# Optimization experiments

Measured on AMD Instinct MI355X. Metric: run time of the kernel, lower is better.

## Reference

```python
import jax, jax.numpy as jnp
import numpy as np

VOCAB = 32000
HID = 1024
CUTOFFS = [0, 10000, 20000, 32000]
N_CLUSTERS = 2
DIV = 4
PROJ_DIMS = [HID // DIV**i for i in range(N_CLUSTERS + 1)]  # [1024, 256, 64]
# Faithful to source quirk: n_vocabs = cutoffs[i] + cutoffs[i+1]
LOGIT_DIMS = [CUTOFFS[i] + CUTOFFS[i + 1] for i in range(N_CLUSTERS + 1)]  # [10000, 30000, 52000]


def setup_inputs() -> dict:
    key = jax.random.key(0)
    ks = jax.random.split(key, 16)
    N = 2048
    inp = {
        "x": jax.random.normal(ks[0], (N, HID), dtype=jnp.float32),
        "y": jax.random.randint(ks[1], (N,), 0, VOCAB, dtype=jnp.int64),
    }
    s = 0.02
    # projections: Linear(hidden, proj_dims[i], bias=False); stored as [in, out]
    inp["Wp0"] = jax.random.normal(ks[2], (HID, PROJ_DIMS[0]), dtype=jnp.float32) * s
    inp["Wp1"] = jax.random.normal(ks[3], (HID, PROJ_DIMS[1]), dtype=jnp.float32) * s
    inp["Wp2"] = jax.random.normal(ks[4], (HID, PROJ_DIMS[2]), dtype=jnp.float32) * s
    # logits: Linear(proj_dims[i], LOGIT_DIMS[i]) with bias
    inp["Wl0"] = jax.random.normal(ks[5], (PROJ_DIMS[0], LOGIT_DIMS[0]), dtype=jnp.float32) * s
    inp["bl0"] = jnp.zeros((LOGIT_DIMS[0],), dtype=jnp.float32)
    inp["Wl1"] = jax.random.normal(ks[6], (PROJ_DIMS[1], LOGIT_DIMS[1]), dtype=jnp.float32) * s
    inp["bl1"] = jnp.zeros((LOGIT_DIMS[1],), dtype=jnp.float32)
    inp["Wl2"] = jax.random.normal(ks[7], (PROJ_DIMS[2], LOGIT_DIMS[2]), dtype=jnp.float32) * s
    inp["bl2"] = jnp.zeros((LOGIT_DIMS[2],), dtype=jnp.float32)
    # cluster_logit: Linear(hidden, n_clusters)
    inp["Wc"] = jax.random.normal(ks[8], (HID, N_CLUSTERS), dtype=jnp.float32) * s
    inp["bc"] = jnp.zeros((N_CLUSTERS,), dtype=jnp.float32)
    return inp


def reference(x, y, Wp0, Wp1, Wp2, Wl0, bl0, Wl1, bl1, Wl2, bl2, Wc, bc):
    # head: project (dim-preserving here) then head-vocab logits + cluster logits
    head_proj = x @ Wp0                                   # [N, 1024]
    head_logit = jnp.concatenate(
        [head_proj @ Wl0 + bl0, head_proj @ Wc + bc], axis=1
    )                                                     # [N, 10000 + 2]
    head_lp = jax.nn.log_softmax(head_logit, axis=1)

    nll = jnp.zeros(y.shape, dtype=x.dtype)

    # cluster 0: targets in [0, cutoffs[1])
    m0 = (y >= CUTOFFS[0]) & (y < CUTOFFS[1])
    t0 = jnp.clip(y - CUTOFFS[0], 0, head_lp.shape[1] - 1)
    lp0 = jnp.take_along_axis(head_lp, t0[:, None], axis=1)[:, 0]
    nll = jnp.where(m0, -lp0, nll)

    # tail clusters: small projection GEMM + log_softmax + gather, combined via masks
    tails = [(Wp1, Wl1, bl1), (Wp2, Wl2, bl2)]
    for i, (Wp, Wl, bl) in enumerate(tails, start=1):
        l, r = CUTOFFS[i], CUTOFFS[i + 1]
        mask = (y >= l) & (y < r)
        t = jnp.clip(y - l, 0, Wl.shape[1] - 1)
        tail_lp = jax.nn.log_softmax((x @ Wp) @ Wl + bl, axis=1)  # [N, LOGIT_DIMS[i]]
        # faithful to source: head column -i (reversed cluster order quirk)
        lp = head_lp[:, -i] + jnp.take_along_axis(tail_lp, t[:, None], axis=1)[:, 0]
        nll = jnp.where(mask, -lp, nll)

    return nll
```

## Files before the change

kernel.cpp:

```cpp
#include <hip/hip_runtime.h>
#include <math.h>

#define HID 1024
#define NROWS 2048

typedef __attribute__((ext_vector_type(8))) short short8;
typedef __attribute__((ext_vector_type(4))) short short4_t;
typedef __attribute__((ext_vector_type(4))) float f32x4;

__device__ __forceinline__ short f2bf(float f) {
  union { float f; unsigned u; } v; v.f = f;
  unsigned r = v.u + 0x7fffu + ((v.u >> 16) & 1u);
  return (short)(r >> 16);
}
__device__ __forceinline__ float bf2f(short s) {
  union { unsigned u; float f; } v; v.u = ((unsigned)(unsigned short)s) << 16;
  return v.f;
}
__device__ __forceinline__ float wave_sum(float a) {
#pragma unroll
  for (int off = 32; off; off >>= 1) a += __shfl_xor(a, off, 64);
  return a;
}

__global__ __launch_bounds__(256) void prep(
    const float* __restrict__ x, const int* __restrict__ y,
    const float* __restrict__ Wp0, const float* __restrict__ Wp1,
    const float* __restrict__ Wp2, const float* __restrict__ Wl0,
    const float* __restrict__ Wl1, const float* __restrict__ Wl2,
    short* __restrict__ xb,
    int* __restrict__ counts, int* __restrict__ slot_of_row,
    int* __restrict__ rows1, int* __restrict__ rows2,
    short* __restrict__ T0, short* __restrict__ T1, short* __restrict__ T2,
    short* __restrict__ T3, short* __restrict__ T4, short* __restrict__ T5) {
  const int tid = threadIdx.x;
  int b = blockIdx.x;
  if (b == 0) {
    __shared__ int c1s, c2s;
    if (tid == 0) { c1s = 0; c2s = 0; }
    __syncthreads();
    for (int r = tid; r < NROWS; r += 256) {
      const int yy = y[r];
      if (yy >= 20000) {
        const int s = atomicAdd(&c2s, 1);
        slot_of_row[r] = s; rows2[s] = r;
      } else if (yy >= 10000) {
        const int s = atomicAdd(&c1s, 1);
        slot_of_row[r] = s; rows1[s] = r;
      } else {
        slot_of_row[r] = -1;
      }
    }
    __syncthreads();
    if (tid == 0) { counts[0] = NROWS; counts[1] = c1s; counts[2] = c2s; }
    return;
  }
  if (b <= 2048) {
    const int i = ((b - 1) * 256 + tid) * 4;
    short4_t o;
    o.x = f2bf(x[i + 0]); o.y = f2bf(x[i + 1]);
    o.z = f2bf(x[i + 2]); o.w = f2bf(x[i + 3]);
    *(short4_t*)&xb[i] = o;
    return;
  }
  b -= 2049;
  const float* W; short* BT; int K, N, Npad, tn;
  if (b < 1024)                { W = Wp0; BT = T0; K = 1024; N = 1024;  Npad = 1024;  tn = 32;   }
  else if ((b -= 1024) < 256)  { W = Wp1; BT = T1; K = 1024; N = 256;   Npad = 256;   tn = 8;    }
  else if ((b -= 256) < 128)   { W = Wp2; BT = T2; K = 1024; N = 64;    Npad = 128;   tn = 4;    }
  else if ((b -= 128) < 10112) { W = Wl0; BT = T3; K = 1024; N = 10000; Npad = 10112; tn = 316;  }
  else if ((b -= 10112) < 7520){ W = Wl1; BT = T4; K = 256;  N = 30000; Npad = 30080; tn = 940;  }
  else { b -= 7520;              W = Wl2; BT = T5; K = 64;   N = 52000; Npad = 52096; tn = 1628; }

  __shared__ float T[32][33];
  const int n0 = (b % tn) * 32, k0 = (b / tn) * 32;
  const int r = tid >> 3, c = (tid & 7) * 4;
  float v0 = 0.f, v1 = 0.f, v2 = 0.f, v3 = 0.f;
  const float* p = &W[(size_t)(k0 + r) * N];
  if (n0 + c + 3 < N) {
    v0 = p[n0 + c]; v1 = p[n0 + c + 1]; v2 = p[n0 + c + 2]; v3 = p[n0 + c + 3];
  } else {
    if (n0 + c + 0 < N) v0 = p[n0 + c + 0];
    if (n0 + c + 1 < N) v1 = p[n0 + c + 1];
    if (n0 + c + 2 < N) v2 = p[n0 + c + 2];
  }
  T[r][c] = v0; T[r][c + 1] = v1; T[r][c + 2] = v2; T[r][c + 3] = v3;
  __syncthreads();
  const int nl = tid >> 3, kl = (tid & 7) * 4;
  const int n = n0 + nl;
  if (n < Npad) {
    short4_t o;
    o.x = (n < N) ? f2bf(T[kl + 0][nl]) : (short)0;
    o.y = (n < N) ? f2bf(T[kl + 1][nl]) : (short)0;
    o.z = (n < N) ? f2bf(T[kl + 2][nl]) : (short)0;
    o.w = (n < N) ? f2bf(T[kl + 3][nl]) : (short)0;
    *(short4_t*)&BT[(size_t)n * K + k0 + kl] = o;
  }
}

__device__ __forceinline__ void mfma_mainloop(const short* aB[4], const short* bB[4],
                                              short* As, short* Bs,
                                              f32x4 acc[4][4],
                                              int K, int w, int lane) {
  const int quad = lane >> 4, ln = lane & 15;
  const int wm = w >> 1, wn = w & 1;
  const int l7 = ln & 7;
  for (int kt = 0; kt < K; kt += 64) {
#pragma unroll
    for (int i = 0; i < 4; ++i) {
      const int row = w * 32 + i * 8;
      __builtin_amdgcn_global_load_lds(
          (const __attribute__((address_space(1))) void*)(aB[i] + kt),
          (__attribute__((address_space(3))) void*)(As + row * 64), 16, 0, 0);
      __builtin_amdgcn_global_load_lds(
          (const __attribute__((address_space(1))) void*)(bB[i] + kt),
          (__attribute__((address_space(3))) void*)(Bs + row * 64), 16, 0, 0);
    }
    __syncthreads();
#pragma unroll
    for (int ks = 0; ks < 2; ++ks) {
      const int kcs = ks * 4 + quad;
      short8 af[4], bfr[4];
#pragma unroll
      for (int mt = 0; mt < 4; ++mt) {
        const int row = wm * 64 + mt * 16 + ln;
        af[mt] = *(const short8*)(As + ((row * 8 + (kcs ^ l7)) << 3));
      }
#pragma unroll
      for (int nt = 0; nt < 4; ++nt) {
        const int rowb = wn * 64 + nt * 16 + ln;
        bfr[nt] = *(const short8*)(Bs + ((rowb * 8 + (kcs ^ l7)) << 3));
      }
#pragma unroll
      for (int mt = 0; mt < 4; ++mt)
#pragma unroll
        for (int nt = 0; nt < 4; ++nt)
          acc[mt][nt] = __builtin_amdgcn_mfma_f32_16x16x32_bf16(
              af[mt], bfr[nt], acc[mt][nt], 0, 0, 0);
    }
    __syncthreads();
  }
}


__global__ __launch_bounds__(256) void proj_all(
    const short* __restrict__ xb,
    const short* __restrict__ WpT0, const short* __restrict__ WpT1,
    const short* __restrict__ WpT2,
    short* __restrict__ P0b, short* __restrict__ P1c, short* __restrict__ P2c,
    const int* __restrict__ rows1, const int* __restrict__ rows2,
    const int* __restrict__ counts) {
  int b = blockIdx.x;
  const short* BT; short* C; int N, r0, c0, cnt;
  const int* rowlist = nullptr;
  if (b < 128) {
    BT = WpT0; C = P0b; N = 1024;
    c0 = (b & 7) * 128; r0 = (b >> 3) * 128; cnt = NROWS;
  } else if (b < 160) {
    b -= 128; BT = WpT1; C = P1c; N = 256;
    c0 = (b & 1) * 128; r0 = (b >> 1) * 128; rowlist = rows1; cnt = counts[1];
  } else {
    b -= 160; BT = WpT2; C = P2c; N = 64;
    c0 = 0; r0 = b * 128; rowlist = rows2; cnt = counts[2];
  }
  if (r0 >= cnt) return;

  __shared__ short As[128 * 64];
  __shared__ short Bs[128 * 64];
  const int tid = threadIdx.x;
  const int w = tid >> 6, lane = tid & 63;
  const int quad = lane >> 4, ln = lane & 15;
  const int wm = w >> 1, wn = w & 1;
  const int rsub = lane >> 3;
  const int kc = (lane & 7) ^ rsub;
  const int K = 1024;

  const short* aB[4]; const short* bB[4];
#pragma unroll
  for (int i = 0; i < 4; ++i) {
    const int sl = r0 + w * 32 + i * 8 + rsub;
    const int ar = rowlist ? rowlist[sl < cnt ? sl : cnt - 1] : sl;
    aB[i] = xb + (size_t)ar * K + kc * 8;
    bB[i] = BT + (size_t)(c0 + w * 32 + i * 8 + rsub) * K + kc * 8;
  }

  f32x4 acc[4][4];
  const f32x4 zero = {0.f, 0.f, 0.f, 0.f};
#pragma unroll
  for (int i = 0; i < 4; ++i)
#pragma unroll
    for (int j = 0; j < 4; ++j) acc[i][j] = zero;
  mfma_mainloop(aB, bB, As, Bs, acc, K, w, lane);
#pragma unroll
  for (int mt = 0; mt < 4; ++mt)
#pragma unroll
    for (int r = 0; r < 4; ++r) {
      const int grow = r0 + wm * 64 + mt * 16 + quad * 4 + r;
#pragma unroll
      for (int nt = 0; nt < 4; ++nt) {
        const int cg = c0 + wn * 64 + nt * 16 + ln;
        if (cg < N) C[(size_t)grow * N + cg] = f2bf(acc[mt][nt][r]);
      }
    }
}

#define HB  1280
#define T1B 3840
#define T2B 6528

__global__ __launch_bounds__(256) void logit_all(
    const short* __restrict__ P0b, const short* __restrict__ WlT0,
    const float* __restrict__ bl0, float* __restrict__ psh,
    const short* __restrict__ P1c, const short* __restrict__ WlT1,
    const float* __restrict__ bl1, float* __restrict__ ps1,
    const short* __restrict__ P2c, const short* __restrict__ WlT2,
    const float* __restrict__ bl2, float* __restrict__ ps2,
    const int* __restrict__ counts) {
  int b = blockIdx.x;
  const short* A; const short* BT; const float* bias; float* ps;
  int K, Ncols, nsplit, rb, cs, cnt;
  if (b < HB) {
    const int xcd = b & 7, j = b >> 3;
    rb = j / 10; cs = xcd * 10 + j % 10;
    if (cs >= 79) return;
    A = P0b; BT = WlT0; bias = bl0; ps = psh;
    K = 1024; Ncols = 10000; nsplit = 79; cnt = NROWS;
  } else if ((b -= HB) < T1B) {
    const int xcd = b & 7, j = b >> 3;
    rb = j / 30; cs = xcd * 30 + j % 30;
    if (cs >= 235) return;
    A = P1c; BT = WlT1; bias = bl1; ps = ps1;
    K = 256; Ncols = 30000; nsplit = 235; cnt = counts[1];
  } else {
    b -= T1B;
    const int xcd = b & 7, j = b >> 3;
    rb = j / 51; cs = xcd * 51 + j % 51;
    if (cs >= 407) return;
    A = P2c; BT = WlT2; bias = bl2; ps = ps2;
    K = 64; Ncols = 52000; nsplit = 407; cnt = counts[2];
  }
  const int r0 = rb * 128, c0 = cs * 128;
  if (r0 >= cnt) return;

  __shared__ short As[128 * 64];
  __shared__ short Bs[128 * 64];
  __shared__ float psL[2][128];
  const int tid = threadIdx.x;
  const int w = tid >> 6, lane = tid & 63;
  const int quad = lane >> 4, ln = lane & 15;
  const int wm = w >> 1, wn = w & 1;
  const int rsub = lane >> 3;
  const int kc = (lane & 7) ^ rsub;

  const short* aB[4]; const short* bB[4];
#pragma unroll
  for (int i = 0; i < 4; ++i) {
    aB[i] = A + (size_t)(r0 + w * 32 + i * 8 + rsub) * K + kc * 8;
    bB[i] = BT + (size_t)(c0 + w * 32 + i * 8 + rsub) * K + kc * 8;
  }

  f32x4 acc[4][4];
  const f32x4 zero = {0.f, 0.f, 0.f, 0.f};
#pragma unroll
  for (int i = 0; i < 4; ++i)
#pragma unroll
    for (int j = 0; j < 4; ++j) acc[i][j] = zero;
  mfma_mainloop(aB, bB, As, Bs, acc, K, w, lane);

  float bv[4];
#pragma unroll
  for (int nt = 0; nt < 4; ++nt) {
    const int cg = c0 + wn * 64 + nt * 16 + ln;
    bv[nt] = (cg < Ncols) ? bias[cg] : -1.0e30f;
  }
#pragma unroll
  for (int mt = 0; mt < 4; ++mt)
#pragma unroll
    for (int r = 0; r < 4; ++r) {
      float s = 0.f;
#pragma unroll
      for (int nt = 0; nt < 4; ++nt)
        s += __expf(acc[mt][nt][r] + bv[nt]);
#pragma unroll
      for (int off = 1; off < 16; off <<= 1) s += __shfl_xor(s, off, 64);
      if (ln == 0) psL[wn][wm * 64 + mt * 16 + quad * 4 + r] = s;
    }
  __syncthreads();
  if (tid < 128)
    ps[(size_t)(r0 + tid) * nsplit + cs] = psL[0][tid] + psL[1][tid];
}

__global__ __launch_bounds__(256) void finalize(
    const short* __restrict__ P0b, const short* __restrict__ P1c,
    const short* __restrict__ P2c,
    const short* __restrict__ WlT0, const float* __restrict__ bl0,
    const short* __restrict__ WlT1, const float* __restrict__ bl1,
    const short* __restrict__ WlT2, const float* __restrict__ bl2,
    const float* __restrict__ Wc, const float* __restrict__ bc,
    const int* __restrict__ y, const int* __restrict__ slot_of_row,
    const float* __restrict__ psh, const float* __restrict__ ps1,
    const float* __restrict__ ps2, float* __restrict__ out) {
  const int lane = threadIdx.x & 63;
  const int row = blockIdx.x * 4 + (threadIdx.x >> 6);

  float a0 = 0.f, a1 = 0.f;
  for (int k = lane; k < HID; k += 64) {
    const float p = bf2f(P0b[(size_t)row * HID + k]);
    a0 += p * Wc[2 * k];
    a1 += p * Wc[2 * k + 1];
  }
  a0 = wave_sum(a0);
  a1 = wave_sum(a1);
  const float cl0 = a0 + bc[0], cl1 = a1 + bc[1];

  float S = 0.f;
  for (int i = lane; i < 79; i += 64) S += psh[(size_t)row * 79 + i];
  S = wave_sum(S) + __expf(cl0) + __expf(cl1);
  const float lse = logf(S);

  const int yy = y[row];
  float nll;
  if (yy < 10000) {
    const short* pr = P0b + (size_t)row * 1024;
    const short* wr = WlT0 + (size_t)yy * 1024;
    float a = 0.f;
    for (int kk = lane * 4; kk < 1024; kk += 256) {
      const short4_t p = *(const short4_t*)(pr + kk);
      const short4_t wv = *(const short4_t*)(wr + kk);
      a += bf2f(p.x) * bf2f(wv.x) + bf2f(p.y) * bf2f(wv.y)
         + bf2f(p.z) * bf2f(wv.z) + bf2f(p.w) * bf2f(wv.w);
    }
    a = wave_sum(a);
    nll = -((a + bl0[yy]) - lse);
  } else if (yy < 20000) {
    const int t = yy - 10000;
    const int slot = slot_of_row[row];
    float S1 = 0.f;
    for (int i = lane; i < 235; i += 64) S1 += ps1[(size_t)slot * 235 + i];
    S1 = wave_sum(S1);
    const short* pr = P1c + (size_t)slot * 256;
    const short* wr = WlT1 + (size_t)t * 256;
    const int kk = lane * 4;
    const short4_t p = *(const short4_t*)(pr + kk);
    const short4_t wv = *(const short4_t*)(wr + kk);
    float a = bf2f(p.x) * bf2f(wv.x) + bf2f(p.y) * bf2f(wv.y)
            + bf2f(p.z) * bf2f(wv.z) + bf2f(p.w) * bf2f(wv.w);
    a = wave_sum(a);
    nll = -((cl1 - lse) + ((a + bl1[t]) - logf(S1)));
  } else {
    const int t = yy - 20000;
    const int slot = slot_of_row[row];
    float S2 = 0.f;
    for (int i = lane; i < 407; i += 64) S2 += ps2[(size_t)slot * 407 + i];
    S2 = wave_sum(S2);
    float a = 0.f;
    if (lane < 16) {
      const short* pr = P2c + (size_t)slot * 64;
      const short* wr = WlT2 + (size_t)t * 64;
      const int kk = lane * 4;
      const short4_t p = *(const short4_t*)(pr + kk);
      const short4_t wv = *(const short4_t*)(wr + kk);
      a = bf2f(p.x) * bf2f(wv.x) + bf2f(p.y) * bf2f(wv.y)
        + bf2f(p.z) * bf2f(wv.z) + bf2f(p.w) * bf2f(wv.w);
    }
    a = wave_sum(a);
    nll = -((cl0 - lse) + ((a + bl2[t]) - logf(S2)));
  }
  if (lane == 0) out[row] = nll;
}

extern "C" void kernel_launch(void* const* d_in, const int* in_sizes, int n_in,
                              void* d_out, int out_size, void* d_ws, size_t ws_size,
                              hipStream_t stream) {
  const float* x   = (const float*)d_in[0];
  const int*   y   = (const int*)d_in[1];
  const float* Wp0 = (const float*)d_in[2];
  const float* Wp1 = (const float*)d_in[3];
  const float* Wp2 = (const float*)d_in[4];
  const float* Wl0 = (const float*)d_in[5];
  const float* bl0 = (const float*)d_in[6];
  const float* Wl1 = (const float*)d_in[7];
  const float* bl1 = (const float*)d_in[8];
  const float* Wl2 = (const float*)d_in[9];
  const float* bl2 = (const float*)d_in[10];
  const float* Wc  = (const float*)d_in[11];
  const float* bc  = (const float*)d_in[12];
  float* out = (float*)d_out;

  float* fws = (float*)d_ws;
  float* psh = fws; fws += (size_t)NROWS * 79;
  float* ps1 = fws; fws += (size_t)NROWS * 235;
  float* ps2 = fws; fws += (size_t)NROWS * 407;
  int* iws = (int*)fws;
  int* counts      = iws; iws += 4;
  int* slot_of_row = iws; iws += NROWS;
  int* rows1       = iws; iws += NROWS;
  int* rows2       = iws; iws += NROWS;
  short* sp = (short*)iws;
  short* xb   = sp; sp += (size_t)NROWS * 1024;
  short* P0b  = sp; sp += (size_t)NROWS * 1024;
  short* P1c  = sp; sp += (size_t)NROWS * 256;
  short* P2c  = sp; sp += (size_t)NROWS * 64;
  short* WpT0 = sp; sp += (size_t)1024 * 1024;
  short* WpT1 = sp; sp += (size_t)256 * 1024;
  short* WpT2 = sp; sp += (size_t)128 * 1024;
  short* WlT0 = sp; sp += (size_t)10112 * 1024;
  short* WlT1 = sp; sp += (size_t)30080 * 256;
  short* WlT2 = sp; sp += (size_t)52096 * 64;

  dim3 blk(256);
  prep<<<dim3(24345), blk, 0, stream>>>(x, y, Wp0, Wp1, Wp2, Wl0, Wl1, Wl2,
                                        xb, counts, slot_of_row, rows1, rows2,
                                        WpT0, WpT1, WpT2, WlT0, WlT1, WlT2);
  proj_all<<<dim3(176), blk, 0, stream>>>(xb, WpT0, WpT1, WpT2, P0b, P1c, P2c,
                                          rows1, rows2, counts);
  logit_all<<<dim3(HB + T1B + T2B), blk, 0, stream>>>(
      P0b, WlT0, bl0, psh, P1c, WlT1, bl1, ps1, P2c, WlT2, bl2, ps2, counts);
  finalize<<<dim3(NROWS / 4), blk, 0, stream>>>(
      P0b, P1c, P2c, WlT0, bl0, WlT1, bl1, WlT2, bl2, Wc, bc, y, slot_of_row,
      psh, ps1, ps2, out);
}
```

Measured before the change: 310.2 us.

## Split head logit GEMM into dedicated 256x256 tiled kernel with direct-to-LDS loads

Moves the 2048x10000x1024 head logit GEMM out of the shared logit kernel into its own 512-thread kernel. The new kernel uses 256x256 tiles, global_load_lds asynchronous staging into double-buffered LDS, and an interleaved schedule of barriers and MFMAs with setprio. The head weight transpose is padded to 10240 columns so the larger tiles divide it evenly. The goal is higher MFMA utilisation and more data reuse on the dominant GEMM. The costs are an extra kernel launch, 128KB of LDS per block, and only 320 blocks, which may leave some CUs underfilled.

Result: no change. 304.8 us (-1.7%).

```diff
diff --git a/kernel.cpp b/kernel.cpp
--- a/kernel.cpp
+++ b/kernel.cpp
@@ -68,8 +68,8 @@
   if (b < 1024)                { W = Wp0; BT = T0; K = 1024; N = 1024;  Npad = 1024;  tn = 32;   }
   else if ((b -= 1024) < 256)  { W = Wp1; BT = T1; K = 1024; N = 256;   Npad = 256;   tn = 8;    }
   else if ((b -= 256) < 128)   { W = Wp2; BT = T2; K = 1024; N = 64;    Npad = 128;   tn = 4;    }
-  else if ((b -= 128) < 10112) { W = Wl0; BT = T3; K = 1024; N = 10000; Npad = 10112; tn = 316;  }
-  else if ((b -= 10112) < 7520){ W = Wl1; BT = T4; K = 256;  N = 30000; Npad = 30080; tn = 940;  }
+  else if ((b -= 128) < 10240) { W = Wl0; BT = T3; K = 1024; N = 10000; Npad = 10240; tn = 320;  }
+  else if ((b -= 10240) < 7520){ W = Wl1; BT = T4; K = 256;  N = 30000; Npad = 30080; tn = 940;  }
   else { b -= 7520;              W = Wl2; BT = T5; K = 64;   N = 52000; Npad = 52096; tn = 1628; }
 
   __shared__ float T[32][33];
@@ -204,13 +204,159 @@
     }
 }
 
-#define HB  1280
+#define GLOAD_LDS(g, l)                                                      \
+  __builtin_amdgcn_global_load_lds(                                          \
+      (const __attribute__((address_space(1))) void*)(g),                    \
+      (__attribute__((address_space(3))) void*)(l), 16, 0, 0)
+
+#define BARR do { asm volatile("" ::: "memory");                             \
+                  __builtin_amdgcn_s_barrier();                              \
+                  asm volatile("" ::: "memory"); } while (0)
+
+__device__ __forceinline__ void stage_half(const short* __restrict__ src,
+                                           size_t row0, int kOff,
+                                           short* dst, int w, int rsub, int kc) {
+  const short* g0 = src + (row0 + (size_t)(w * 8 + rsub)) * 1024 + kOff + kc * 8;
+  GLOAD_LDS(g0, dst + w * 512);
+  GLOAD_LDS(g0 + (size_t)64 * 1024, dst + 4096 + w * 512);
+}
+
+#define RD_A(QM) do {                                                        \
+  _Pragma("unroll") for (int mt = 0; mt < 4; ++mt) {                         \
+    const int rL = ((QM) * 4 + mt) * 16 + ln;                                \
+    _Pragma("unroll") for (int kk = 0; kk < 2; ++kk) {                       \
+      const int kcs = kk * 4 + quad;                                         \
+      aq[mt * 2 + kk] = *(const short8*)(Ah + rL * 64 + ((kcs ^ l7) << 3));  \
+    } } } while (0)
+
+#define RD_B(NH) do {                                                        \
+  _Pragma("unroll") for (int nt = 0; nt < 2; ++nt) {                         \
+    const int ntp = (NH) * 2 + nt;                                           \
+    const int cL = cB + ntp * 16 + ln;                                       \
+    _Pragma("unroll") for (int kk = 0; kk < 2; ++kk) {                       \
+      const int kcs = kk * 4 + quad;                                         \
+      bq[ntp * 2 + kk] = *(const short8*)(Bh + cL * 64 + ((kcs ^ l7) << 3)); \
+    } } } while (0)
+
+#define MFMA_Q(QM, QN) do {                                                  \
+  __builtin_amdgcn_s_setprio(1);                                             \
+  _Pragma("unroll") for (int mt = 0; mt < 4; ++mt)                           \
+  _Pragma("unroll") for (int nt = 0; nt < 2; ++nt)                           \
+  _Pragma("unroll") for (int kk = 0; kk < 2; ++kk)                           \
+    acc[(QM) * 4 + mt][(QN) * 2 + nt] =                                      \
+        __builtin_amdgcn_mfma_f32_16x16x32_bf16(                             \
+            aq[mt * 2 + kk], bq[((QN) * 2 + nt) * 2 + kk],                   \
+            acc[(QM) * 4 + mt][(QN) * 2 + nt], 0, 0, 0);                     \
+  __builtin_amdgcn_s_setprio(0);                                             \
+} while (0)
+
+__global__ __launch_bounds__(512, 2) void logit_head(
+    const short* __restrict__ P0b, const short* __restrict__ WlT0,
+    const float* __restrict__ bl0, float* __restrict__ psh) {
+  const int b = blockIdx.x;
+  const int xcd = b & 7, j = b >> 3;
+  const int cb = xcd * 5 + j % 5, rb = j / 5;
+  const int r0 = rb * 256;
+  const size_t c0 = (size_t)cb * 256;
+
+  __shared__ short lds[65536];
+  short* const Abase = lds;
+  short* const Bbase = lds + 32768;
+
+  const int tid = threadIdx.x;
+  const int w = tid >> 6, lane = tid & 63;
+  const int quad = lane >> 4, ln = lane & 15, l7 = lane & 7;
+  const int wm = w >> 2, wn = w & 3;
+  const int rsub = lane >> 3, kc = (lane & 7) ^ rsub;
+  const int cB = (wn & 1) * 64;
+
+  stage_half(P0b, (size_t)r0,        0,  Abase,          w, rsub, kc);
+  stage_half(P0b, (size_t)r0 + 128,  0,  Abase + 8192,   w, rsub, kc);
+  stage_half(WlT0, c0,               0,  Bbase,          w, rsub, kc);
+  stage_half(WlT0, c0 + 128,         0,  Bbase + 8192,   w, rsub, kc);
+  stage_half(WlT0, c0,               64, Bbase + 16384,  w, rsub, kc);
+  stage_half(WlT0, c0 + 128,         64, Bbase + 24576,  w, rsub, kc);
+  asm volatile("s_waitcnt vmcnt(4)" ::: "memory");
+  __builtin_amdgcn_s_barrier();
+  asm volatile("" ::: "memory");
+
+  f32x4 acc[8][4];
+  const f32x4 zero = {0.f, 0.f, 0.f, 0.f};
+#pragma unroll
+  for (int i = 0; i < 8; ++i)
+#pragma unroll
+    for (int jj = 0; jj < 4; ++jj) acc[i][jj] = zero;
+
+  short8 aq[8], bq[8];
+  const short* const Ard = Abase + wm * 8192;
+  const short* const Brd = Bbase + (wn >> 1) * 8192;
+
+#pragma unroll 2
+  for (int u = 0; u < 16; ++u) {
+    const int c = u & 1;
+    const short* Ah = Ard + c * 16384;
+    const short* Bh = Brd + c * 16384;
+    short* An = Abase + (c ^ 1) * 16384;
+    short* Bn = Bbase + c * 16384;
+    const int k1 = (u + 1) << 6, k2 = (u + 2) << 6;
+
+    RD_A(0);
+    RD_B(0);
+    if (u < 15) stage_half(P0b, (size_t)r0, k1, An, w, rsub, kc);
+    BARR;
+    MFMA_Q(0, 0);
+    BARR;
+    RD_B(1);
+    if (u < 15) stage_half(P0b, (size_t)r0 + 128, k1, An + 8192, w, rsub, kc);
+    BARR;
+    MFMA_Q(0, 1);
+    BARR;
+    RD_A(1);
+    if (u < 14) stage_half(WlT0, c0, k2, Bn, w, rsub, kc);
+    BARR;
+    MFMA_Q(1, 0);
+    BARR;
+    if (u < 14) stage_half(WlT0, c0 + 128, k2, Bn + 8192, w, rsub, kc);
+    BARR;
+    MFMA_Q(1, 1);
+    if (u < 14) { asm volatile("s_waitcnt vmcnt(4)" ::: "memory"); }
+    else        { asm volatile("s_waitcnt vmcnt(0)" ::: "memory"); }
+    BARR;
+  }
+
+  float bv[4];
+#pragma unroll
+  for (int nt = 0; nt < 4; ++nt) {
+    const size_t cg = c0 + (size_t)wn * 64 + nt * 16 + ln;
+    bv[nt] = (cg < 10000) ? bl0[cg] : -1.0e30f;
+  }
+  float* psL = (float*)lds;
+#pragma unroll
+  for (int mt = 0; mt < 8; ++mt)
+#pragma unroll
+    for (int r = 0; r < 4; ++r) {
+      float s = 0.f;
+#pragma unroll
+      for (int nt = 0; nt < 4; ++nt) s += __expf(acc[mt][nt][r] + bv[nt]);
+#pragma unroll
+      for (int off = 1; off < 16; off <<= 1) s += __shfl_xor(s, off, 64);
+      if (ln == 0)
+        psL[(wn & 1) * 512 + (wn >> 1) * 256 + wm * 128 + mt * 16 + quad * 4 + r] = s;
+    }
+  BARR;
+  {
+    const int sL = tid >> 8, rowL = tid & 255;
+    const int csg = (int)(c0 >> 7) + sL;
+    if (csg < 79)
+      psh[(size_t)(r0 + rowL) * 79 + csg] =
+          psL[sL * 256 + rowL] + psL[512 + sL * 256 + rowL];
+  }
+}
+
 #define T1B 3840
 #define T2B 6528
 
-__global__ __launch_bounds__(256) void logit_all(
-    const short* __restrict__ P0b, const short* __restrict__ WlT0,
-    const float* __restrict__ bl0, float* __restrict__ psh,
+__global__ __launch_bounds__(256) void logit_tails(
     const short* __restrict__ P1c, const short* __restrict__ WlT1,
     const float* __restrict__ bl1, float* __restrict__ ps1,
     const short* __restrict__ P2c, const short* __restrict__ WlT2,
@@ -219,13 +365,7 @@
   int b = blockIdx.x;
   const short* A; const short* BT; const float* bias; float* ps;
   int K, Ncols, nsplit, rb, cs, cnt;
-  if (b < HB) {
-    const int xcd = b & 7, j = b >> 3;
-    rb = j / 10; cs = xcd * 10 + j % 10;
-    if (cs >= 79) return;
-    A = P0b; BT = WlT0; bias = bl0; ps = psh;
-    K = 1024; Ncols = 10000; nsplit = 79; cnt = NROWS;
-  } else if ((b -= HB) < T1B) {
+  if (b < T1B) {
     const int xcd = b & 7, j = b >> 3;
     rb = j / 30; cs = xcd * 30 + j % 30;
     if (cs >= 235) return;
@@ -264,7 +404,7 @@
 #pragma unroll
   for (int i = 0; i < 4; ++i)
 #pragma unroll
-    for (int j = 0; j < 4; ++j) acc[i][j] = zero;
+    for (int jj = 0; jj < 4; ++jj) acc[i][jj] = zero;
   mfma_mainloop(aB, bB, As, Bs, acc, K, w, lane);
 
   float bv[4];
@@ -404,18 +544,19 @@
   short* WpT0 = sp; sp += (size_t)1024 * 1024;
   short* WpT1 = sp; sp += (size_t)256 * 1024;
   short* WpT2 = sp; sp += (size_t)128 * 1024;
-  short* WlT0 = sp; sp += (size_t)10112 * 1024;
+  short* WlT0 = sp; sp += (size_t)10240 * 1024;
   short* WlT1 = sp; sp += (size_t)30080 * 256;
   short* WlT2 = sp; sp += (size_t)52096 * 64;
 
   dim3 blk(256);
-  prep<<<dim3(24345), blk, 0, stream>>>(x, y, Wp0, Wp1, Wp2, Wl0, Wl1, Wl2,
+  prep<<<dim3(24473), blk, 0, stream>>>(x, y, Wp0, Wp1, Wp2, Wl0, Wl1, Wl2,
                                         xb, counts, slot_of_row, rows1, rows2,
                                         WpT0, WpT1, WpT2, WlT0, WlT1, WlT2);
   proj_all<<<dim3(176), blk, 0, stream>>>(xb, WpT0, WpT1, WpT2, P0b, P1c, P2c,
                                           rows1, rows2, counts);
-  logit_all<<<dim3(HB + T1B + T2B), blk, 0, stream>>>(
-      P0b, WlT0, bl0, psh, P1c, WlT1, bl1, ps1, P2c, WlT2, bl2, ps2, counts);
+  logit_tails<<<dim3(T1B + T2B), blk, 0, stream>>>(
+      P1c, WlT1, bl1, ps1, P2c, WlT2, bl2, ps2, counts);
+  logit_head<<<dim3(320), dim3(512), 0, stream>>>(P0b, WlT0, bl0, psh);
   finalize<<<dim3(NROWS / 4), blk, 0, stream>>>(
       P0b, P1c, P2c, WlT0, bl0, WlT1, bl1, WlT2, bl2, Wc, bc, y, slot_of_row,
       psh, ps1, ps2, out);
```

## Rewrite logit GEMM kernel with 256x256 pipelined head tiles and A-reuse tail loops

Applied to the files above, without the earlier changes.

Replaces the 128x128-tile logit kernel with a 512-thread kernel. The head GEMM now uses 256x256 tiles, double-buffered LDS staging and staged barriers that interleave loads with MFMA quadrants. The tail clusters keep the A tile resident in LDS while looping over several column blocks, and cluster 2 double-buffers its B tiles. WlT0 padding grows to 10240 columns to fit the wider tiles. The aim is more reuse per load and fewer blocks and launches, at the cost of 64K-short LDS and register pressure, with tighter occupancy under launch_bounds(512,2).

New measurement: 431.1 us. +38.9%, slower.

```diff
diff --git a/kernel.cpp b/kernel.cpp
--- a/kernel.cpp
+++ b/kernel.cpp
@@ -68,8 +68,8 @@
   if (b < 1024)                { W = Wp0; BT = T0; K = 1024; N = 1024;  Npad = 1024;  tn = 32;   }
   else if ((b -= 1024) < 256)  { W = Wp1; BT = T1; K = 1024; N = 256;   Npad = 256;   tn = 8;    }
   else if ((b -= 256) < 128)   { W = Wp2; BT = T2; K = 1024; N = 64;    Npad = 128;   tn = 4;    }
-  else if ((b -= 128) < 10112) { W = Wl0; BT = T3; K = 1024; N = 10000; Npad = 10112; tn = 316;  }
-  else if ((b -= 10112) < 7520){ W = Wl1; BT = T4; K = 256;  N = 30000; Npad = 30080; tn = 940;  }
+  else if ((b -= 128) < 10240) { W = Wl0; BT = T3; K = 1024; N = 10000; Npad = 10240; tn = 320;  }
+  else if ((b -= 10240) < 7520){ W = Wl1; BT = T4; K = 256;  N = 30000; Npad = 30080; tn = 940;  }
   else { b -= 7520;              W = Wl2; BT = T5; K = 64;   N = 52000; Npad = 52096; tn = 1628; }
 
   __shared__ float T[32][33];
@@ -97,6 +97,48 @@
     *(short4_t*)&BT[(size_t)n * K + k0 + kl] = o;
   }
 }
+
+#define GLOAD_LDS(g, l)                                                      \
+  __builtin_amdgcn_global_load_lds(                                          \
+      (const __attribute__((address_space(1))) void*)(g),                    \
+      (__attribute__((address_space(3))) void*)(l), 16, 0, 0)
+
+#define BARR do { asm volatile("" ::: "memory");                             \
+                  __builtin_amdgcn_s_barrier();                              \
+                  asm volatile("" ::: "memory"); } while (0)
+
+__device__ __forceinline__ void stage_half(const short* __restrict__ src,
+                                           size_t row0, int kOff, short* dst,
+                                           int stride, int w, int rsub, int kc) {
+  const short* g0 = src + (row0 + (size_t)(w * 8 + rsub)) * (size_t)stride
+                    + kOff + kc * 8;
+  GLOAD_LDS(g0, dst + w * 512);
+  GLOAD_LDS(g0 + (size_t)64 * stride, dst + 4096 + w * 512);
+}
+
+#define RD_A8(dst, base) do {                                                \
+  _Pragma("unroll") for (int mt = 0; mt < 4; ++mt)                           \
+  _Pragma("unroll") for (int kk = 0; kk < 2; ++kk)                           \
+    dst[mt * 2 + kk] = *(const short8*)((base) +                             \
+        (pm * 64 + mt * 16 + ln) * 64 + (((kk * 4 + quad) ^ l7) << 3));      \
+} while (0)
+
+#define RD_B4(dst, base) do {                                                \
+  _Pragma("unroll") for (int nt = 0; nt < 2; ++nt)                           \
+  _Pragma("unroll") for (int kk = 0; kk < 2; ++kk)                           \
+    dst[nt * 2 + kk] = *(const short8*)((base) +                             \
+        (pn * 32 + nt * 16 + ln) * 64 + (((kk * 4 + quad) ^ l7) << 3));      \
+} while (0)
+
+#define MFMA16(ACC, ar, br) do {                                             \
+  __builtin_amdgcn_s_setprio(1);                                             \
+  _Pragma("unroll") for (int mt = 0; mt < 4; ++mt)                           \
+  _Pragma("unroll") for (int nt = 0; nt < 2; ++nt)                           \
+  _Pragma("unroll") for (int kk = 0; kk < 2; ++kk)                           \
+    ACC[mt][nt] = __builtin_amdgcn_mfma_f32_16x16x32_bf16(                   \
+        ar[mt * 2 + kk], br[nt * 2 + kk], ACC[mt][nt], 0, 0, 0);             \
+  __builtin_amdgcn_s_setprio(0);                                             \
+} while (0)
 
 __device__ __forceinline__ void mfma_mainloop(const short* aB[4], const short* bB[4],
                                               short* As, short* Bs,
@@ -204,11 +246,7 @@
     }
 }
 
-#define HB  1280
-#define T1B 3840
-#define T2B 6528
-
-__global__ __launch_bounds__(256) void logit_all(
+__global__ __launch_bounds__(512, 2) void logit_fused(
     const short* __restrict__ P0b, const short* __restrict__ WlT0,
     const float* __restrict__ bl0, float* __restrict__ psh,
     const short* __restrict__ P1c, const short* __restrict__ WlT1,
@@ -216,78 +254,217 @@
     const short* __restrict__ P2c, const short* __restrict__ WlT2,
     const float* __restrict__ bl2, float* __restrict__ ps2,
     const int* __restrict__ counts) {
-  int b = blockIdx.x;
-  const short* A; const short* BT; const float* bias; float* ps;
-  int K, Ncols, nsplit, rb, cs, cnt;
-  if (b < HB) {
-    const int xcd = b & 7, j = b >> 3;
-    rb = j / 10; cs = xcd * 10 + j % 10;
-    if (cs >= 79) return;
-    A = P0b; BT = WlT0; bias = bl0; ps = psh;
-    K = 1024; Ncols = 10000; nsplit = 79; cnt = NROWS;
-  } else if ((b -= HB) < T1B) {
-    const int xcd = b & 7, j = b >> 3;
-    rb = j / 30; cs = xcd * 30 + j % 30;
-    if (cs >= 235) return;
-    A = P1c; BT = WlT1; bias = bl1; ps = ps1;
-    K = 256; Ncols = 30000; nsplit = 235; cnt = counts[1];
-  } else {
-    b -= T1B;
-    const int xcd = b & 7, j = b >> 3;
-    rb = j / 51; cs = xcd * 51 + j % 51;
-    if (cs >= 407) return;
-    A = P2c; BT = WlT2; bias = bl2; ps = ps2;
-    K = 64; Ncols = 52000; nsplit = 407; cnt = counts[2];
-  }
-  const int r0 = rb * 128, c0 = cs * 128;
-  if (r0 >= cnt) return;
-
-  __shared__ short As[128 * 64];
-  __shared__ short Bs[128 * 64];
-  __shared__ float psL[2][128];
+  __shared__ short lds[65536];
+  __shared__ float psE[4][2][256];
   const int tid = threadIdx.x;
   const int w = tid >> 6, lane = tid & 63;
-  const int quad = lane >> 4, ln = lane & 15;
-  const int wm = w >> 1, wn = w & 1;
-  const int rsub = lane >> 3;
-  const int kc = (lane & 7) ^ rsub;
-
-  const short* aB[4]; const short* bB[4];
-#pragma unroll
-  for (int i = 0; i < 4; ++i) {
-    aB[i] = A + (size_t)(r0 + w * 32 + i * 8 + rsub) * K + kc * 8;
-    bB[i] = BT + (size_t)(c0 + w * 32 + i * 8 + rsub) * K + kc * 8;
-  }
-
-  f32x4 acc[4][4];
-  const f32x4 zero = {0.f, 0.f, 0.f, 0.f};
-#pragma unroll
-  for (int i = 0; i < 4; ++i)
-#pragma unroll
-    for (int j = 0; j < 4; ++j) acc[i][j] = zero;
-  mfma_mainloop(aB, bB, As, Bs, acc, K, w, lane);
-
-  float bv[4];
-#pragma unroll
-  for (int nt = 0; nt < 4; ++nt) {
-    const int cg = c0 + wn * 64 + nt * 16 + ln;
-    bv[nt] = (cg < Ncols) ? bias[cg] : -1.0e30f;
-  }
-#pragma unroll
-  for (int mt = 0; mt < 4; ++mt)
-#pragma unroll
-    for (int r = 0; r < 4; ++r) {
-      float s = 0.f;
-#pragma unroll
-      for (int nt = 0; nt < 4; ++nt)
-        s += __expf(acc[mt][nt][r] + bv[nt]);
-#pragma unroll
-      for (int off = 1; off < 16; off <<= 1) s += __shfl_xor(s, off, 64);
-      if (ln == 0) psL[wn][wm * 64 + mt * 16 + quad * 4 + r] = s;
-    }
-  __syncthreads();
-  if (tid < 128)
-    ps[(size_t)(r0 + tid) * nsplit + cs] = psL[0][tid] + psL[1][tid];
+  const int quad = lane >> 4, ln = lane & 15, l7 = lane & 7;
+  const int pm = w >> 2, pn = w & 3;
+  const int rsub = lane >> 3, kc = (lane & 7) ^ rsub;
+  const int b = blockIdx.x;
+
+  if (b < 320) {
+    const int xcd = b & 7, j = b >> 3;
+    const int cb = xcd * 5 + j % 5, rb = j / 5;
+    const int r0 = rb * 256;
+    const size_t c0 = (size_t)cb * 256;
+    short* const Abase = lds;
+    short* const Bbase = lds + 32768;
+
+    stage_half(P0b, (size_t)r0,        0,  Abase,          1024, w, rsub, kc);
+    stage_half(P0b, (size_t)r0 + 128,  0,  Abase + 8192,   1024, w, rsub, kc);
+    stage_half(WlT0, c0,               0,  Bbase,          1024, w, rsub, kc);
+    stage_half(WlT0, c0 + 128,         0,  Bbase + 8192,   1024, w, rsub, kc);
+    stage_half(P0b, (size_t)r0,        64, Abase + 16384,  1024, w, rsub, kc);
+    stage_half(P0b, (size_t)r0 + 128,  64, Abase + 24576,  1024, w, rsub, kc);
+    stage_half(WlT0, c0,               64, Bbase + 16384,  1024, w, rsub, kc);
+    stage_half(WlT0, c0 + 128,         64, Bbase + 24576,  1024, w, rsub, kc);
+
+    f32x4 acc[2][2][4][2];
+    const f32x4 zero = {0.f, 0.f, 0.f, 0.f};
+#pragma unroll
+    for (int qa = 0; qa < 2; ++qa)
+#pragma unroll
+      for (int qb = 0; qb < 2; ++qb)
+#pragma unroll
+        for (int mt = 0; mt < 4; ++mt)
+#pragma unroll
+          for (int nt = 0; nt < 2; ++nt) acc[qa][qb][mt][nt] = zero;
+
+#pragma unroll 2
+    for (int u = 0; u < 16; ++u) {
+      const int cc = u & 1;
+      short* const Ab = Abase + cc * 16384;
+      short* const Bb = Bbase + cc * 16384;
+      const int k2 = (u + 2) << 6;
+      short8 aq0[8], aq1[8], bq0[4], bq1[4];
+      if (u < 15) { asm volatile("s_waitcnt vmcnt(8)" ::: "memory"); }
+      else        { asm volatile("s_waitcnt vmcnt(0)" ::: "memory"); }
+      __builtin_amdgcn_s_barrier();
+      asm volatile("" ::: "memory");
+      RD_A8(aq0, Ab);
+      RD_B4(bq0, Bb);
+      MFMA16(acc[0][0], aq0, bq0);
+      BARR;
+      if (u < 14) {
+        stage_half(P0b, (size_t)r0, k2, Ab, 1024, w, rsub, kc);
+        stage_half(WlT0, c0, k2, Bb, 1024, w, rsub, kc);
+      }
+      RD_B4(bq1, Bb + 8192);
+      MFMA16(acc[0][1], aq0, bq1);
+      BARR;
+      if (u < 14) stage_half(WlT0, c0 + 128, k2, Bb + 8192, 1024, w, rsub, kc);
+      RD_A8(aq1, Ab + 8192);
+      MFMA16(acc[1][1], aq1, bq1);
+      BARR;
+      if (u < 14) stage_half(P0b, (size_t)r0 + 128, k2, Ab + 8192, 1024, w, rsub, kc);
+      MFMA16(acc[1][0], aq1, bq0);
+    }
+
+    float bv[2][2];
+#pragma unroll
+    for (int qb = 0; qb < 2; ++qb)
+#pragma unroll
+      for (int nt = 0; nt < 2; ++nt) {
+        const size_t cg = c0 + qb * 128 + pn * 32 + nt * 16 + ln;
+        bv[qb][nt] = (cg < 10000) ? bl0[cg] : -1.0e30f;
+      }
+#pragma unroll
+    for (int qa = 0; qa < 2; ++qa)
+#pragma unroll
+      for (int qb = 0; qb < 2; ++qb)
+#pragma unroll
+        for (int mt = 0; mt < 4; ++mt)
+#pragma unroll
+          for (int r = 0; r < 4; ++r) {
+            float s = __expf(acc[qa][qb][mt][0][r] + bv[qb][0]) +
+                      __expf(acc[qa][qb][mt][1][r] + bv[qb][1]);
+#pragma unroll
+            for (int off = 1; off < 16; off <<= 1) s += __shfl_xor(s, off, 64);
+            if (ln == 0)
+              psE[pn][qb][qa * 128 + pm * 64 + mt * 16 + quad * 4 + r] = s;
+          }
+    BARR;
+    {
+      const int qb = tid >> 8, row = tid & 255;
+      const int cs = cb * 2 + qb;
+      if (cs < 79)
+        psh[(size_t)(r0 + row) * 79 + cs] =
+            psE[0][qb][row] + psE[1][qb][row] + psE[2][qb][row] + psE[3][qb][row];
+    }
+    return;
+  }
+
+  if (b < 800) {
+    const int b1 = b - 320;
+    const int grp = b1 >> 4, rb = b1 & 15;
+    const int r0 = rb * 128;
+    if (r0 >= counts[1]) return;
+    const int cs0 = grp * 8;
+    short* const As = lds;
+    short* const Bs = lds + 32768;
+#pragma unroll
+    for (int kt = 0; kt < 4; ++kt)
+      stage_half(P1c, (size_t)r0, kt * 64, As + kt * 8192, 256, w, rsub, kc);
+    for (int g = 0; g < 8; ++g) {
+      const int cs = cs0 + g;
+      if (cs >= 235) break;
+#pragma unroll
+      for (int kt = 0; kt < 4; ++kt)
+        stage_half(WlT1, (size_t)cs * 128, kt * 64, Bs + kt * 8192, 256, w, rsub, kc);
+      asm volatile("s_waitcnt vmcnt(0)" ::: "memory");
+      __builtin_amdgcn_s_barrier();
+      asm volatile("" ::: "memory");
+      f32x4 acc[4][2];
+      const f32x4 zero = {0.f, 0.f, 0.f, 0.f};
+#pragma unroll
+      for (int mt = 0; mt < 4; ++mt)
+#pragma unroll
+        for (int nt = 0; nt < 2; ++nt) acc[mt][nt] = zero;
+#pragma unroll
+      for (int kt = 0; kt < 4; ++kt) {
+        short8 a_[8], b_[4];
+        RD_A8(a_, As + kt * 8192);
+        RD_B4(b_, Bs + kt * 8192);
+        MFMA16(acc, a_, b_);
+      }
+      float bv[2];
+#pragma unroll
+      for (int nt = 0; nt < 2; ++nt) {
+        const int cg = cs * 128 + pn * 32 + nt * 16 + ln;
+        bv[nt] = (cg < 30000) ? bl1[cg] : -1.0e30f;
+      }
+#pragma unroll
+      for (int mt = 0; mt < 4; ++mt)
+#pragma unroll
+        for (int r = 0; r < 4; ++r) {
+          float s = __expf(acc[mt][0][r] + bv[0]) + __expf(acc[mt][1][r] + bv[1]);
+#pragma unroll
+          for (int off = 1; off < 16; off <<= 1) s += __shfl_xor(s, off, 64);
+          if (ln == 0) psE[pn][0][pm * 64 + mt * 16 + quad * 4 + r] = s;
+        }
+      BARR;
+      if (tid < 128)
+        ps1[(size_t)(r0 + tid) * 235 + cs] =
+            psE[0][0][tid] + psE[1][0][tid] + psE[2][0][tid] + psE[3][0][tid];
+    }
+    return;
+  }
+
+  {
+    const int b2 = b - 800;
+    const int grp = b2 >> 4, rb = b2 & 15;
+    const int r0 = rb * 128;
+    if (r0 >= counts[2]) return;
+    const int cs0 = grp * 16;
+    short* const As = lds;
+    short* const Bbuf0 = lds + 8192;
+    short* const Bbuf1 = lds + 16384;
+    stage_half(P2c, (size_t)r0, 0, As, 64, w, rsub, kc);
+    stage_half(WlT2, (size_t)cs0 * 128, 0, Bbuf0, 64, w, rsub, kc);
+    for (int g = 0; g < 16; ++g) {
+      const int cs = cs0 + g;
+      if (cs >= 407) break;
+      const bool more = (g < 15) && (cs + 1 < 407);
+      if (more)
+        stage_half(WlT2, (size_t)(cs + 1) * 128, 0, (g & 1) ? Bbuf0 : Bbuf1,
+                   64, w, rsub, kc);
+      if (more) { asm volatile("s_waitcnt vmcnt(2)" ::: "memory"); }
+      else      { asm volatile("s_waitcnt vmcnt(0)" ::: "memory"); }
+      __builtin_amdgcn_s_barrier();
+      asm volatile("" ::: "memory");
+      short8 a_[8], b_[4];
+      RD_A8(a_, As);
+      RD_B4(b_, (g & 1) ? Bbuf1 : Bbuf0);
+      f32x4 acc[4][2];
+      const f32x4 zero = {0.f, 0.f, 0.f, 0.f};
+#pragma unroll
+      for (int mt = 0; mt < 4; ++mt)
+#pragma unroll
+        for (int nt = 0; nt < 2; ++nt) acc[mt][nt] = zero;
+      MFMA16(acc, a_, b_);
+      float bv[2];
+#pragma unroll
+      for (int nt = 0; nt < 2; ++nt) {
+        const int cg = cs * 128 + pn * 32 + nt * 16 + ln;
+        bv[nt] = (cg < 52000) ? bl2[cg] : -1.0e30f;
+      }
+#pragma unroll
+      for (int mt = 0; mt < 4; ++mt)
+#pragma unroll
+        for (int r = 0; r < 4; ++r) {
+          float s = __expf(acc[mt][0][r] + bv[0]) + __expf(acc[mt][1][r] + bv[1]);
+#pragma unroll
+          for (int off = 1; off < 16; off <<= 1) s += __shfl_xor(s, off, 64);
+          if (ln == 0) psE[pn][0][pm * 64 + mt * 16 + quad * 4 + r] = s;
+        }
+      BARR;
+      if (tid < 128)
+        ps2[(size_t)(r0 + tid) * 407 + cs] =
+            psE[0][0][tid] + psE[1][0][tid] + psE[2][0][tid] + psE[3][0][tid];
+    }
+    return;
+  }
 }
 
 __global__ __launch_bounds__(256) void finalize(
@@ -404,17 +581,17 @@
   short* WpT0 = sp; sp += (size_t)1024 * 1024;
   short* WpT1 = sp; sp += (size_t)256 * 1024;
   short* WpT2 = sp; sp += (size_t)128 * 1024;
-  short* WlT0 = sp; sp += (size_t)10112 * 1024;
+  short* WlT0 = sp; sp += (size_t)10240 * 1024;
   short* WlT1 = sp; sp += (size_t)30080 * 256;
   short* WlT2 = sp; sp += (size_t)52096 * 64;
 
   dim3 blk(256);
-  prep<<<dim3(24345), blk, 0, stream>>>(x, y, Wp0, Wp1, Wp2, Wl0, Wl1, Wl2,
+  prep<<<dim3(24473), blk, 0, stream>>>(x, y, Wp0, Wp1, Wp2, Wl0, Wl1, Wl2,
                                         xb, counts, slot_of_row, rows1, rows2,
                                         WpT0, WpT1, WpT2, WlT0, WlT1, WlT2);
   proj_all<<<dim3(176), blk, 0, stream>>>(xb, WpT0, WpT1, WpT2, P0b, P1c, P2c,
                                           rows1, rows2, counts);
-  logit_all<<<dim3(HB + T1B + T2B), blk, 0, stream>>>(
+  logit_fused<<<dim3(1216), dim3(512), 0, stream>>>(
       P0b, WlT0, bl0, psh, P1c, WlT1, bl1, ps1, P2c, WlT2, bl2, ps2, counts);
   finalize<<<dim3(NROWS / 4), blk, 0, stream>>>(
       P0b, P1c, P2c, WlT0, bl0, WlT1, bl1, WlT2, bl2, Wc, bc, y, slot_of_row,
```

## Replace logit GEMM with 256x256-tile double-buffered 8-wave pipelined kernel

Applied to the files above, without the earlier changes.

Swaps the 128x128 logit GEMM for a 512-thread kernel that computes 256x256 tiles as four quadrants. It double-buffers LDS with async global-to-LDS loads interleaved between MFMA groups, using explicit vmcnt waits, raw barriers and setprio. The transposed logit weights are padded to multiples of 256 so whole tiles can be staged. The aim is more data reuse per loaded byte and overlap of memory with MFMA, at the cost of 128KB LDS per block, more registers and fragile hand-written synchronisation.

Measured after the change: 318.3 us. +2.6%, slower.

```diff
diff --git a/kernel.cpp b/kernel.cpp
--- a/kernel.cpp
+++ b/kernel.cpp
@@ -68,9 +68,9 @@
   if (b < 1024)                { W = Wp0; BT = T0; K = 1024; N = 1024;  Npad = 1024;  tn = 32;   }
   else if ((b -= 1024) < 256)  { W = Wp1; BT = T1; K = 1024; N = 256;   Npad = 256;   tn = 8;    }
   else if ((b -= 256) < 128)   { W = Wp2; BT = T2; K = 1024; N = 64;    Npad = 128;   tn = 4;    }
-  else if ((b -= 128) < 10112) { W = Wl0; BT = T3; K = 1024; N = 10000; Npad = 10112; tn = 316;  }
-  else if ((b -= 10112) < 7520){ W = Wl1; BT = T4; K = 256;  N = 30000; Npad = 30080; tn = 940;  }
-  else { b -= 7520;              W = Wl2; BT = T5; K = 64;   N = 52000; Npad = 52096; tn = 1628; }
+  else if ((b -= 128) < 10240) { W = Wl0; BT = T3; K = 1024; N = 10000; Npad = 10240; tn = 320;  }
+  else if ((b -= 10240) < 7552){ W = Wl1; BT = T4; K = 256;  N = 30000; Npad = 30208; tn = 944;  }
+  else { b -= 7552;              W = Wl2; BT = T5; K = 64;   N = 52000; Npad = 52224; tn = 1632; }
 
   __shared__ float T[32][33];
   const int n0 = (b % tn) * 32, k0 = (b / tn) * 32;
@@ -98,6 +98,139 @@
   }
 }
 
+#define GLOAD_LDS(g, l)                                                      \
+  __builtin_amdgcn_global_load_lds(                                          \
+      (const __attribute__((address_space(1))) void*)(g),                    \
+      (__attribute__((address_space(3))) void*)(l), 16, 0, 0)
+
+#define BARR do { asm volatile("" ::: "memory");                             \
+                  __builtin_amdgcn_s_barrier();                              \
+                  asm volatile("" ::: "memory"); } while (0)
+
+#define VMW(n) asm volatile("s_waitcnt vmcnt(" #n ")" ::: "memory")
+
+__device__ __forceinline__ void stage_half(const short* __restrict__ src,
+                                           size_t row0, int kOff, short* dst,
+                                           int stride, int w, int rsub, int kc) {
+  const short* g0 = src + (row0 + (size_t)(w * 8 + rsub)) * (size_t)stride
+                    + kOff + kc * 8;
+  GLOAD_LDS(g0, dst + w * 512);
+  GLOAD_LDS(g0 + (size_t)64 * stride, dst + 4096 + w * 512);
+}
+
+#define RD_A8(dst, base) do {                                                \
+  _Pragma("unroll") for (int mt = 0; mt < 4; ++mt)                           \
+  _Pragma("unroll") for (int kk = 0; kk < 2; ++kk)                           \
+    dst[mt * 2 + kk] = *(const short8*)((base) +                             \
+        (pm * 64 + mt * 16 + ln) * 64 + (((kk * 4 + quad) ^ l7) << 3));      \
+} while (0)
+
+#define RD_B4(dst, base) do {                                                \
+  _Pragma("unroll") for (int nt = 0; nt < 2; ++nt)                           \
+  _Pragma("unroll") for (int kk = 0; kk < 2; ++kk)                           \
+    dst[nt * 2 + kk] = *(const short8*)((base) +                             \
+        (pn * 32 + nt * 16 + ln) * 64 + (((kk * 4 + quad) ^ l7) << 3));      \
+} while (0)
+
+#define MFMA16(ACC, ar, br) do {                                             \
+  __builtin_amdgcn_s_setprio(1);                                             \
+  _Pragma("unroll") for (int mt = 0; mt < 4; ++mt)                           \
+  _Pragma("unroll") for (int nt = 0; nt < 2; ++nt)                           \
+  _Pragma("unroll") for (int kk = 0; kk < 2; ++kk)                           \
+    ACC[mt][nt] = __builtin_amdgcn_mfma_f32_16x16x32_bf16(                   \
+        ar[mt * 2 + kk], br[nt * 2 + kk], ACC[mt][nt], 0, 0, 0);             \
+  __builtin_amdgcn_s_setprio(0);                                             \
+} while (0)
+
+__device__ __forceinline__ void gemm256(
+    const short* __restrict__ A, const short* __restrict__ BT,
+    int K, int NT, size_t rowA0, size_t rowB0, short* lds,
+    f32x4 acc[2][2][4][2], int w, int lane) {
+  const int quad = lane >> 4, ln = lane & 15, l7 = lane & 7;
+  const int pm = w >> 2, pn = w & 3;
+  const int rsub = lane >> 3, kc = (lane & 7) ^ rsub;
+  short* const Abase = lds;
+  short* const Bbase = lds + 32768;
+
+  stage_half(A,  rowA0,       0, Abase,        K, w, rsub, kc);
+  stage_half(BT, rowB0,       0, Bbase,        K, w, rsub, kc);
+  stage_half(BT, rowB0 + 128, 0, Bbase + 8192, K, w, rsub, kc);
+  stage_half(A,  rowA0 + 128, 0, Abase + 8192, K, w, rsub, kc);
+
+  for (int u = 0; u < NT; ++u) {
+    const int c = u & 1;
+    const short* Ah = Abase + c * 16384;
+    const short* Bh = Bbase + c * 16384;
+    short* const An = Abase + (c ^ 1) * 16384;
+    short* const Bn = Bbase + (c ^ 1) * 16384;
+    const int k1 = (u + 1) << 6;
+    const bool more = (u < NT - 1);
+    short8 aq0[8], aq1[8], bq0[4], bq1[4];
+    VMW(4);
+    BARR;
+    RD_A8(aq0, Ah);
+    RD_B4(bq0, Bh);
+    if (more) stage_half(A, rowA0, k1, An, K, w, rsub, kc);
+    MFMA16(acc[0][0], aq0, bq0);
+    if (more) { VMW(4); } else { VMW(2); }
+    BARR;
+    RD_B4(bq1, Bh + 8192);
+    if (more) stage_half(BT, rowB0, k1, Bn, K, w, rsub, kc);
+    MFMA16(acc[0][1], aq0, bq1);
+    if (more) { VMW(4); } else { VMW(0); }
+    BARR;
+    RD_A8(aq1, Ah + 8192);
+    if (more) stage_half(BT, rowB0 + 128, k1, Bn + 8192, K, w, rsub, kc);
+    MFMA16(acc[1][1], aq1, bq1);
+    BARR;
+    if (more) stage_half(A, rowA0 + 128, k1, An + 8192, K, w, rsub, kc);
+    MFMA16(acc[1][0], aq1, bq0);
+  }
+}
+
+
+__device__ __forceinline__ void exp_epilogue(
+    f32x4 acc[2][2][4][2], const float* __restrict__ bias,
+    float* __restrict__ ps, size_t c0, int Ncols, int nsplit, int r0,
+    short* lds, int tid, int w, int lane) {
+  const int quad = lane >> 4, ln = lane & 15;
+  const int pm = w >> 2, pn = w & 3;
+  float bv[2][2];
+#pragma unroll
+  for (int qb = 0; qb < 2; ++qb)
+#pragma unroll
+    for (int nt = 0; nt < 2; ++nt) {
+      const size_t cg = c0 + qb * 128 + pn * 32 + nt * 16 + ln;
+      bv[qb][nt] = (cg < (size_t)Ncols) ? bias[cg] : -1.0e30f;
+    }
+  float* const psF = (float*)lds;
+  BARR;
+#pragma unroll
+  for (int qa = 0; qa < 2; ++qa)
+#pragma unroll
+    for (int qb = 0; qb < 2; ++qb)
+#pragma unroll
+      for (int mt = 0; mt < 4; ++mt)
+#pragma unroll
+        for (int r = 0; r < 4; ++r) {
+          float s = __expf(acc[qa][qb][mt][0][r] + bv[qb][0]) +
+                    __expf(acc[qa][qb][mt][1][r] + bv[qb][1]);
+#pragma unroll
+          for (int off = 1; off < 16; off <<= 1) s += __shfl_xor(s, off, 64);
+          if (ln == 0)
+            psF[(pn * 2 + qb) * 256 + qa * 128 + pm * 64 + mt * 16 + quad * 4 + r] = s;
+        }
+  BARR;
+  {
+    const int qb = tid >> 8, row = tid & 255;
+    const int cs = (int)(c0 >> 7) + qb;
+    if (cs < nsplit)
+      ps[(size_t)(r0 + row) * nsplit + cs] =
+          psF[(0 * 2 + qb) * 256 + row] + psF[(1 * 2 + qb) * 256 + row] +
+          psF[(2 * 2 + qb) * 256 + row] + psF[(3 * 2 + qb) * 256 + row];
+  }
+}
+
 __device__ __forceinline__ void mfma_mainloop(const short* aB[4], const short* bB[4],
                                               short* As, short* Bs,
                                               f32x4 acc[4][4],
@@ -141,7 +274,6 @@
     __syncthreads();
   }
 }
-
 
 __global__ __launch_bounds__(256) void proj_all(
     const short* __restrict__ xb,
@@ -204,11 +336,7 @@
     }
 }
 
-#define HB  1280
-#define T1B 3840
-#define T2B 6528
-
-__global__ __launch_bounds__(256) void logit_all(
+__global__ __launch_bounds__(512, 2) void logit_fused(
     const short* __restrict__ P0b, const short* __restrict__ WlT0,
     const float* __restrict__ bl0, float* __restrict__ psh,
     const short* __restrict__ P1c, const short* __restrict__ WlT1,
@@ -216,78 +344,50 @@
     const short* __restrict__ P2c, const short* __restrict__ WlT2,
     const float* __restrict__ bl2, float* __restrict__ ps2,
     const int* __restrict__ counts) {
-  int b = blockIdx.x;
-  const short* A; const short* BT; const float* bias; float* ps;
-  int K, Ncols, nsplit, rb, cs, cnt;
-  if (b < HB) {
-    const int xcd = b & 7, j = b >> 3;
-    rb = j / 10; cs = xcd * 10 + j % 10;
-    if (cs >= 79) return;
-    A = P0b; BT = WlT0; bias = bl0; ps = psh;
-    K = 1024; Ncols = 10000; nsplit = 79; cnt = NROWS;
-  } else if ((b -= HB) < T1B) {
-    const int xcd = b & 7, j = b >> 3;
-    rb = j / 30; cs = xcd * 30 + j % 30;
-    if (cs >= 235) return;
-    A = P1c; BT = WlT1; bias = bl1; ps = ps1;
-    K = 256; Ncols = 30000; nsplit = 235; cnt = counts[1];
-  } else {
-    b -= T1B;
-    const int xcd = b & 7, j = b >> 3;
-    rb = j / 51; cs = xcd * 51 + j % 51;
-    if (cs >= 407) return;
-    A = P2c; BT = WlT2; bias = bl2; ps = ps2;
-    K = 64; Ncols = 52000; nsplit = 407; cnt = counts[2];
-  }
-  const int r0 = rb * 128, c0 = cs * 128;
-  if (r0 >= cnt) return;
-
-  __shared__ short As[128 * 64];
-  __shared__ short Bs[128 * 64];
-  __shared__ float psL[2][128];
+  __shared__ short lds[65536];
   const int tid = threadIdx.x;
   const int w = tid >> 6, lane = tid & 63;
-  const int quad = lane >> 4, ln = lane & 15;
-  const int wm = w >> 1, wn = w & 1;
-  const int rsub = lane >> 3;
-  const int kc = (lane & 7) ^ rsub;
-
-  const short* aB[4]; const short* bB[4];
-#pragma unroll
-  for (int i = 0; i < 4; ++i) {
-    aB[i] = A + (size_t)(r0 + w * 32 + i * 8 + rsub) * K + kc * 8;
-    bB[i] = BT + (size_t)(c0 + w * 32 + i * 8 + rsub) * K + kc * 8;
-  }
-
-  f32x4 acc[4][4];
+  const int b = blockIdx.x;
+
+  const short* A; const short* BT; const float* bias; float* ps;
+  int K, NT, Ncols, nsplit, r0; size_t c0;
+  if (b < 320) {
+    const int xcd = b & 7, j = b >> 3;
+    const int cb = xcd * 5 + j % 5, rb = j / 5;
+    r0 = rb * 256; c0 = (size_t)cb * 256;
+    A = P0b; BT = WlT0; bias = bl0; ps = psh;
+    K = 1024; NT = 16; Ncols = 10000; nsplit = 79;
+  } else if (b < 1264) {
+    const int b1 = b - 320;
+    const int rb = b1 / 118, cb = b1 % 118;
+    r0 = rb * 256;
+    if (r0 >= counts[1]) return;
+    c0 = (size_t)cb * 256;
+    A = P1c; BT = WlT1; bias = bl1; ps = ps1;
+    K = 256; NT = 4; Ncols = 30000; nsplit = 235;
+  } else {
+    const int b2 = b - 1264;
+    const int rb = b2 / 204, cb = b2 % 204;
+    r0 = rb * 256;
+    if (r0 >= counts[2]) return;
+    c0 = (size_t)cb * 256;
+    A = P2c; BT = WlT2; bias = bl2; ps = ps2;
+    K = 64; NT = 1; Ncols = 52000; nsplit = 407;
+  }
+
+  f32x4 acc[2][2][4][2];
   const f32x4 zero = {0.f, 0.f, 0.f, 0.f};
 #pragma unroll
-  for (int i = 0; i < 4; ++i)
-#pragma unroll
-    for (int j = 0; j < 4; ++j) acc[i][j] = zero;
-  mfma_mainloop(aB, bB, As, Bs, acc, K, w, lane);
-
-  float bv[4];
-#pragma unroll
-  for (int nt = 0; nt < 4; ++nt) {
-    const int cg = c0 + wn * 64 + nt * 16 + ln;
-    bv[nt] = (cg < Ncols) ? bias[cg] : -1.0e30f;
-  }
-#pragma unroll
-  for (int mt = 0; mt < 4; ++mt)
-#pragma unroll
-    for (int r = 0; r < 4; ++r) {
-      float s = 0.f;
-#pragma unroll
-      for (int nt = 0; nt < 4; ++nt)
-        s += __expf(acc[mt][nt][r] + bv[nt]);
-#pragma unroll
-      for (int off = 1; off < 16; off <<= 1) s += __shfl_xor(s, off, 64);
-      if (ln == 0) psL[wn][wm * 64 + mt * 16 + quad * 4 + r] = s;
-    }
-  __syncthreads();
-  if (tid < 128)
-    ps[(size_t)(r0 + tid) * nsplit + cs] = psL[0][tid] + psL[1][tid];
+  for (int qa = 0; qa < 2; ++qa)
+#pragma unroll
+    for (int qb = 0; qb < 2; ++qb)
+#pragma unroll
+      for (int mt = 0; mt < 4; ++mt)
+#pragma unroll
+        for (int nt = 0; nt < 2; ++nt) acc[qa][qb][mt][nt] = zero;
+
+  gemm256(A, BT, K, NT, (size_t)r0, c0, lds, acc, w, lane);
+  exp_epilogue(acc, bias, ps, c0, Ncols, nsplit, r0, lds, tid, w, lane);
 }
 
 __global__ __launch_bounds__(256) void finalize(
@@ -404,17 +504,17 @@
   short* WpT0 = sp; sp += (size_t)1024 * 1024;
   short* WpT1 = sp; sp += (size_t)256 * 1024;
   short* WpT2 = sp; sp += (size_t)128 * 1024;
-  short* WlT0 = sp; sp += (size_t)10112 * 1024;
-  short* WlT1 = sp; sp += (size_t)30080 * 256;
-  short* WlT2 = sp; sp += (size_t)52096 * 64;
+  short* WlT0 = sp; sp += (size_t)10240 * 1024;
+  short* WlT1 = sp; sp += (size_t)30208 * 256;
+  short* WlT2 = sp; sp += (size_t)52224 * 64;
 
   dim3 blk(256);
-  prep<<<dim3(24345), blk, 0, stream>>>(x, y, Wp0, Wp1, Wp2, Wl0, Wl1, Wl2,
+  prep<<<dim3(24513), blk, 0, stream>>>(x, y, Wp0, Wp1, Wp2, Wl0, Wl1, Wl2,
                                         xb, counts, slot_of_row, rows1, rows2,
                                         WpT0, WpT1, WpT2, WlT0, WlT1, WlT2);
   proj_all<<<dim3(176), blk, 0, stream>>>(xb, WpT0, WpT1, WpT2, P0b, P1c, P2c,
                                           rows1, rows2, counts);
-  logit_all<<<dim3(HB + T1B + T2B), blk, 0, stream>>>(
+  logit_fused<<<dim3(2896), dim3(512), 0, stream>>>(
       P0b, WlT0, bl0, psh, P1c, WlT1, bl1, ps1, P2c, WlT2, bl2, ps2, counts);
   finalize<<<dim3(NROWS / 4), blk, 0, stream>>>(
       P0b, P1c, P2c, WlT0, bl0, WlT1, bl1, WlT2, bl2, Wc, bc, y, slot_of_row,
```
